# Kernel optimization log

Measured on AMD Instinct MI355X. Metric: run time of the kernel, lower is better.

The kernel has to match this reference:

```python
import jax, jax.numpy as jnp
import numpy as np

B, CIN, COUT, K, NS, NIN, H = 4, 128, 128, 9, 16384, 16384, 64
W0 = 30.0  # SIREN first-layer frequency


def setup_inputs() -> dict:
    ks = jax.random.split(jax.random.key(0), 8)
    x = jax.random.normal(ks[0], (B, CIN, NIN), dtype=jnp.float32)
    neighbours = jax.random.randint(ks[1], (K, NS), 0, NIN)
    # normalized relative neighbour coordinates in [-1, 1], shape (K*NS, 2)
    coords = 2.0 * jax.random.uniform(ks[2], (K * NS, 2), dtype=jnp.float32) - 1.0
    W1 = jax.random.normal(ks[3], (2, H), dtype=jnp.float32) / jnp.sqrt(2.0)
    b1 = jnp.zeros((H,), dtype=jnp.float32)
    W2 = jax.random.normal(ks[4], (H, H), dtype=jnp.float32) / jnp.sqrt(H * 1.0)
    b2 = jnp.zeros((H,), dtype=jnp.float32)
    W3 = jax.random.normal(ks[5], (H, COUT * CIN), dtype=jnp.float32) / jnp.sqrt(H * 1.0)
    b3 = jnp.zeros((COUT * CIN,), dtype=jnp.float32)
    bias = jnp.zeros((1, COUT, 1), dtype=jnp.float32)
    return {"x": x, "neighbours": neighbours, "coords": coords,
            "W1": W1, "b1": b1, "W2": W2, "b2": b2, "W3": W3, "b3": b3,
            "bias": bias}


def reference(x, neighbours, coords, W1, b1, W2, b2, W3, b3, bias):
    k, ns = neighbours.shape
    cin = x.shape[1]
    cout = W3.shape[1] // cin
    # INR filter generation: (K*NS, 2) -> (K*NS, COUT*CIN)
    h = jnp.sin(W0 * (coords @ W1 + b1))
    h = jnp.sin(h @ W2 + b2)
    f = h @ W3 + b3                                  # (K*NS, COUT*CIN)
    # (K*NS, COUT, CIN) -> (COUT, CIN, K, NS), matching torch permute(1,2,0).reshape
    f = f.reshape(k * ns, cout, cin).transpose(1, 2, 0).reshape(cout, cin, k, ns)
    # neighbor gather: (B, CIN, K, NS)
    x_unfold = x[:, :, neighbours]
    # weighted reduce over (CIN, K) per output location
    out = jnp.einsum('bjkl,ijkl->bil', x_unfold, f)
    return out + bias
```

## Files before the change

### kernel.cpp

```cpp
#include <hip/hip_runtime.h>

#define NS   16384
#define NIN  16384
#define CIN  128
#define COUT 128
#define KNB  9
#define MCH  66
#define QDIM (CIN*MCH)
#define W0C  30.0f

typedef __bf16 bf16;
typedef bf16  bf16x8  __attribute__((ext_vector_type(8)));
typedef bf16  bf16x2  __attribute__((ext_vector_type(2)));
typedef unsigned short u16;
typedef u16   u16x8   __attribute__((ext_vector_type(8)));
typedef float floatx4 __attribute__((ext_vector_type(4)));
typedef unsigned int u32;

__device__ inline u16 f2bf(float f){
  u32 u = __float_as_uint(f);
  u += 0x7fffu + ((u >> 16) & 1u);
  return (u16)(u >> 16);
}
__device__ inline float bf2f(u16 s){
  return __uint_as_float((u32)s << 16);
}
__device__ inline u32 cvtpk2(float lo, float hi){
  u32 r; asm("v_cvt_pk_bf16_f32 %0, %1, %2" : "=v"(r) : "v"(lo), "v"(hi)); return r;
}

#if defined(__has_builtin)
# if __has_builtin(__builtin_amdgcn_fdot2_f32_bf16)
#  define HAVE_DOT2 1
# endif
#endif
#ifndef HAVE_DOT2
# define HAVE_DOT2 0
#endif

__device__ inline float dot2bf(u32 x2, u32 h2, float c){
#if HAVE_DOT2
  return __builtin_amdgcn_fdot2_f32_bf16(__builtin_bit_cast(bf16x2, x2),
                                         __builtin_bit_cast(bf16x2, h2), c, false);
#else
  float xl = bf2f((u16)(x2 & 0xffffu)), xh = bf2f((u16)(x2 >> 16));
  float hl = bf2f((u16)(h2 & 0xffffu)), hh = bf2f((u16)(h2 >> 16));
  return fmaf(xh, hh, fmaf(xl, hl, c));
#endif
}

#define WG_BARRIER() do { \
  asm volatile("s_waitcnt lgkmcnt(0)" ::: "memory"); \
  __builtin_amdgcn_s_barrier(); \
} while (0)

#define PREP_K1H  (NS/32)
#define PREP_KTR  2048
#define PREP_K0   ((COUT*QDIM + 1023)/1024)
__global__ __launch_bounds__(1024) void k_prep(
      const float* __restrict__ coords,
      const float* __restrict__ W1, const float* __restrict__ b1,
      const float* __restrict__ W2, const float* __restrict__ b2,
      const float* __restrict__ x,
      const float* __restrict__ W3, const float* __restrict__ b3,
      u32* __restrict__ hK, u16* __restrict__ xT, u16* __restrict__ Vt){
  __shared__ u16 sh[KNB][32][66];
  __shared__ __align__(16) float tfl[4][32][33];
  const int bid = blockIdx.x;
  const int tid = threadIdx.x;

  if (bid < PREP_K1H){
    const int lane = tid & 63;
    const int w    = tid >> 6;
    const int l0   = bid*32;
    for (int e = w; e < KNB*32; e += 16){
      int k = e >> 5, l = e & 31;
      int pt = (k << 14) + l0 + l;
      float c0 = coords[2*pt], c1 = coords[2*pt+1];
      float z  = fmaf(c0, W1[lane], fmaf(c1, W1[64+lane], b1[lane]));
      float h1 = sinf(W0C * z);
      float acc = b2[lane];
      #pragma unroll
      for (int mp = 0; mp < 64; ++mp)
        acc = fmaf(__shfl(h1, mp, 64), W2[mp*64 + lane], acc);
      sh[k][l][lane] = f2bf(sinf(acc));
      if (lane == 0){ sh[k][l][64] = 0x3F80; sh[k][l][65] = 0; }
    }
    __syncthreads();
    for (int e = tid; e < 66*5*32; e += 1024){
      int m  = e / 160;
      int r  = e - m*160;
      int kp = r >> 5;
      int l  = r & 31;
      u32 lo = sh[2*kp][l][m];
      u32 hi = (kp < 4) ? (u32)sh[2*kp+1][l][m] : 0u;
      hK[(((size_t)m*5 + kp) << 14) + l0 + l] = lo | (hi << 16);
    }
  } else if (bid < PREP_K1H + PREP_KTR){
    const int sub = tid >> 8;
    const int tx  = tid & 31;
    const int ty  = (tid >> 5) & 7;
    const int t   = (bid - PREP_K1H)*4 + sub;
    const int p0  = (t & 511) * 32;
    const int j0  = ((t >> 9) & 3) * 32;
    const int b   = t >> 11;
    const float* xb  = x  + (size_t)b*CIN*NIN;
    u16*         xTb = xT + (size_t)b*NIN*CIN;
    #pragma unroll
    for (int n = 0; n < 4; ++n)
      tfl[sub][ty+8*n][tx] = xb[(size_t)(j0+ty+8*n)*NIN + p0+tx];
    __syncthreads();
    #pragma unroll
    for (int n = 0; n < 4; ++n)
      xTb[(size_t)(p0+ty+8*n)*CIN + j0+tx] = f2bf(tfl[sub][tx][ty+8*n]);
  } else {
    int idx = (bid - PREP_K1H - PREP_KTR)*1024 + tid;
    if (idx < COUT*QDIM){
      int i = idx / QDIM;
      int q = idx - i*QDIM;
      int m = q >> 7;
      int j = q & 127;
      float v = 0.f;
      if (m < 64)       v = W3[m*16384 + i*128 + j];
      else if (m == 64) v = b3[i*128 + j];
      Vt[idx] = f2bf(v);
    }
  }
}

__global__ __launch_bounds__(512, 4) void k_fused(
      const u16* __restrict__ xT,
      const u32* __restrict__ hK,
      const int* __restrict__ nb,
      const u16* __restrict__ Vt,
      const float* __restrict__ bias,
      float* __restrict__ out){
  __shared__ __align__(16) u16 A[2][2][32][136];
  __shared__ u32 hs[2][2][5][32];
  __shared__ int pk[KNB][32];

  const int tid = threadIdx.x;
  const int r0  = blockIdx.x * 32;
  const int b   = r0 >> 14;
  const int l0  = r0 & (NS-1);

  if (tid < KNB*32){
    int k = tid >> 5, l = tid & 31;
    pk[k][l] = nb[k*NS + l0 + l];
  }
  WG_BARRIER();

  const int lq = tid >> 4;
  const int jc = tid & 15;

  const bool hact = tid < 320;
  const int  hs_  = tid / 160;
  const int  hr_  = tid - hs_*160;
  const int  hkp_ = hr_ >> 5;
  const int  hl_  = hr_ & 31;
  const u32* hKp  = hK + (((size_t)(5*hs_ + hkp_)) << 14) + l0 + hl_;
  const size_t HSTR = (size_t)10 << 14;
  u32 hra = 0, hrb = 0;
  if (hact){
    u32 h0 = hKp[0];
    hra = hKp[HSTR];
    hrb = hKp[2*HSTR];
    hs[0][hs_][hkp_][hl_] = h0;
  }

  const char* xbB = (const char*)(xT + ((size_t)b << 21));
  u32 xp[5][8];
  #pragma unroll
  for (int kp = 0; kp < 4; ++kp){
    u16x8 ga = *(const u16x8*)(xbB + (((size_t)(u32)pk[2*kp  ][lq]) << 8) + (size_t)jc*16);
    u16x8 gb = *(const u16x8*)(xbB + (((size_t)(u32)pk[2*kp+1][lq]) << 8) + (size_t)jc*16);
    #pragma unroll
    for (int j = 0; j < 8; ++j) xp[kp][j] = (u32)ga[j] | ((u32)gb[j] << 16);
  }
  {
    u16x8 ga = *(const u16x8*)(xbB + (((size_t)(u32)pk[8][lq]) << 8) + (size_t)jc*16);
    #pragma unroll
    for (int j = 0; j < 8; ++j) xp[4][j] = (u32)ga[j];
  }

  const int lane  = tid & 63;
  const int w     = tid >> 6;
  const int iq    = w & 3;
  const int kh    = w >> 2;
  const int ar    = lane & 15;
  const int klane = lane >> 4;

  floatx4 acc[2][2];
  #pragma unroll
  for (int r = 0; r < 2; ++r)
    #pragma unroll
    for (int f = 0; f < 2; ++f)
      acc[r][f] = (floatx4){0.f,0.f,0.f,0.f};

  const char* VtB0 = (const char*)Vt + (size_t)(iq*32      + ar)*(QDIM*2) + (size_t)(kh*128 + klane*16);
  const char* VtB1 = (const char*)Vt + (size_t)(iq*32 + 16 + ar)*(QDIM*2) + (size_t)(kh*128 + klane*16);

  bf16x8 bv[2][4];
  #pragma unroll
  for (int mm = 0; mm < 2; ++mm)
    #pragma unroll
    for (int kt = 0; kt < 2; ++kt){
      bv[0][mm*2+kt] = *(const bf16x8*)(VtB0 + mm*256 + kt*64);
      bv[1][mm*2+kt] = *(const bf16x8*)(VtB1 + mm*256 + kt*64);
    }

  WG_BARRIER();

  for (int mg = 0; mg < 33; ++mg){
    const int pb = mg & 1;

    float a2[2][8];
    #pragma unroll
    for (int s = 0; s < 2; ++s)
      #pragma unroll
      for (int j = 0; j < 8; ++j) a2[s][j] = 0.f;
    #pragma unroll
    for (int s = 0; s < 2; ++s){
      #pragma unroll
      for (int kp = 0; kp < 5; ++kp){
        u32 hp = hs[pb][s][kp][lq];
        #pragma unroll
        for (int j = 0; j < 8; ++j)
          a2[s][j] = dot2bf(xp[kp][j], hp, a2[s][j]);
      }
    }
    {
      uint4 q0, q1;
      q0.x = cvtpk2(a2[0][0], a2[0][1]); q0.y = cvtpk2(a2[0][2], a2[0][3]);
      q0.z = cvtpk2(a2[0][4], a2[0][5]); q0.w = cvtpk2(a2[0][6], a2[0][7]);
      q1.x = cvtpk2(a2[1][0], a2[1][1]); q1.y = cvtpk2(a2[1][2], a2[1][3]);
      q1.z = cvtpk2(a2[1][4], a2[1][5]); q1.w = cvtpk2(a2[1][6], a2[1][7]);
      *(uint4*)&A[pb][0][lq][jc*8] = q0;
      *(uint4*)&A[pb][1][lq][jc*8] = q1;
    }

    if (hact){
      if (mg < 32) hs[pb^1][hs_][hkp_][hl_] = hra;
      hra = hrb;
      if (mg <= 29) hrb = hKp[(size_t)(mg+3)*HSTR];
    }

    WG_BARRIER();

    #pragma unroll
    for (int mm = 0; mm < 2; ++mm){
      const char* Ab = (const char*)&A[pb][mm][0][0] + kh*128 + klane*16;
      #pragma unroll
      for (int kt = 0; kt < 2; ++kt){
        bf16x8 av0 = *(const bf16x8*)(Ab + (     ar)*272 + kt*64);
        bf16x8 av1 = *(const bf16x8*)(Ab + (16 + ar)*272 + kt*64);
        acc[0][0] = __builtin_amdgcn_mfma_f32_16x16x32_bf16(av0, bv[0][mm*2+kt], acc[0][0], 0, 0, 0);
        acc[0][1] = __builtin_amdgcn_mfma_f32_16x16x32_bf16(av0, bv[1][mm*2+kt], acc[0][1], 0, 0, 0);
        acc[1][0] = __builtin_amdgcn_mfma_f32_16x16x32_bf16(av1, bv[0][mm*2+kt], acc[1][0], 0, 0, 0);
        acc[1][1] = __builtin_amdgcn_mfma_f32_16x16x32_bf16(av1, bv[1][mm*2+kt], acc[1][1], 0, 0, 0);
      }
    }

    if (mg < 32){
      const char* Vg0 = VtB0 + (size_t)(mg+1)*512;
      const char* Vg1 = VtB1 + (size_t)(mg+1)*512;
      #pragma unroll
      for (int mm = 0; mm < 2; ++mm)
        #pragma unroll
        for (int kt = 0; kt < 2; ++kt){
          bv[0][mm*2+kt] = *(const bf16x8*)(Vg0 + mm*256 + kt*64);
          bv[1][mm*2+kt] = *(const bf16x8*)(Vg1 + mm*256 + kt*64);
        }
    }
  }

  WG_BARRIER();
  floatx4* red = (floatx4*)&A[0][0][0][0];
  if (kh == 1){
    floatx4* dst = red + (((size_t)iq*64 + lane) << 2);
    dst[0] = acc[0][0]; dst[1] = acc[0][1]; dst[2] = acc[1][0]; dst[3] = acc[1][1];
  }
  WG_BARRIER();
  if (kh == 0){
    const floatx4* src = red + (((size_t)iq*64 + lane) << 2);
    acc[0][0] += src[0]; acc[0][1] += src[1];
    acc[1][0] += src[2]; acc[1][1] += src[3];
    float* ob = out + ((size_t)b << 21);
    #pragma unroll
    for (int rf = 0; rf < 2; ++rf){
      #pragma unroll
      for (int f = 0; f < 2; ++f){
        int i = iq*32 + f*16 + ar;
        float bi = bias[i];
        int l = l0 + rf*16 + klane*4;
        float4 v;
        v.x = acc[rf][f][0] + bi;
        v.y = acc[rf][f][1] + bi;
        v.z = acc[rf][f][2] + bi;
        v.w = acc[rf][f][3] + bi;
        *(float4*)(ob + ((size_t)i << 14) + l) = v;
      }
    }
  }
}

__global__ __launch_bounds__(256) void k_naive(const float* __restrict__ x,
      const int* __restrict__ nb, const float* __restrict__ coords,
      const float* __restrict__ W1, const float* __restrict__ b1,
      const float* __restrict__ W2, const float* __restrict__ b2,
      const float* __restrict__ W3, const float* __restrict__ b3,
      const float* __restrict__ bias, float* __restrict__ out){
  __shared__ __align__(16) float hk[KNB][68];
  __shared__ int pk[KNB];
  __shared__ __align__(16) float xg[4][KNB][128];
  __shared__ __align__(16) float ul[128][66];
  int tid = threadIdx.x;
  int l = blockIdx.x;
  int lane = tid & 63, wid = tid >> 6;
  if (tid < KNB) pk[tid] = nb[tid*NS + l];
  for (int k = wid; k < KNB; k += 4){
    int pt = k*NS + l;
    float c0 = coords[2*pt], c1 = coords[2*pt+1];
    float z  = fmaf(c0, W1[lane], fmaf(c1, W1[64+lane], b1[lane]));
    float h1 = sinf(W0C*z);
    float a = b2[lane];
    for (int mp = 0; mp < 64; ++mp)
      a = fmaf(__shfl(h1, mp, 64), W2[mp*64+lane], a);
    hk[k][lane] = sinf(a);
    if (lane == 0){ hk[k][64] = 1.f; hk[k][65] = 0.f; }
  }
  __syncthreads();
  for (int idx = tid; idx < 4*KNB*128; idx += 256){
    int b = idx / (KNB*128);
    int r = idx - b*KNB*128;
    int k = r >> 7;
    int j = r & 127;
    xg[b][k][j] = x[((size_t)b*CIN + j)*NIN + pk[k]];
  }
  __syncthreads();
  for (int b = 0; b < 4; ++b){
    for (int idx = tid; idx < 128*65; idx += 256){
      int j = idx / 65, m = idx - j*65;
      float s = 0.f;
      for (int k = 0; k < KNB; ++k) s = fmaf(xg[b][k][j], hk[k][m], s);
      ul[j][m] = s;
    }
    __syncthreads();
    if (tid < 128){
      int i = tid;
      float v = bias[i];
      for (int j = 0; j < 128; ++j){
        const float* wcol = W3 + i*128 + j;
        for (int m = 0; m < 64; ++m)
          v = fmaf(ul[j][m], wcol[(size_t)m*16384], v);
        v = fmaf(ul[j][64], b3[i*128+j], v);
      }
      out[((size_t)b<<21) + ((size_t)i<<14) + l] = v;
    }
    __syncthreads();
  }
}

extern "C" void kernel_launch(void* const* d_in, const int* in_sizes, int n_in,
                              void* d_out, int out_size, void* d_ws, size_t ws_size,
                              hipStream_t stream) {
  const float* x      = (const float*)d_in[0];
  const int*   nb     = (const int*)  d_in[1];
  const float* coords = (const float*)d_in[2];
  const float* W1     = (const float*)d_in[3];
  const float* b1     = (const float*)d_in[4];
  const float* W2     = (const float*)d_in[5];
  const float* b2     = (const float*)d_in[6];
  const float* W3     = (const float*)d_in[7];
  const float* b3     = (const float*)d_in[8];
  const float* bias   = (const float*)d_in[9];
  float* out = (float*)d_out;

  const size_t VT_BYTES = (size_t)COUT*QDIM*2;
  const size_t HK_BYTES = (size_t)MCH*5*NS*4;
  const size_t XT_BYTES = (size_t)4*NIN*CIN*2;
  const size_t FIXED    = VT_BYTES + HK_BYTES + XT_BYTES;

  if (ws_size >= FIXED) {
    char* ws = (char*)d_ws;
    unsigned short* Vt = (unsigned short*)ws;
    u32*            hK = (u32*)(ws + VT_BYTES);
    unsigned short* xT = (unsigned short*)(ws + VT_BYTES + HK_BYTES);

    k_prep<<<PREP_K1H + PREP_KTR + PREP_K0, 1024, 0, stream>>>(
        coords, W1, b1, W2, b2, x, W3, b3, hK, xT, Vt);
    k_fused<<<(4*NS)/32, 512, 0, stream>>>(xT, hK, nb, Vt, bias, out);
  } else {
    k_naive<<<NS, 256, 0, stream>>>(x, nb, coords, W1, b1, W2, b2, W3, b3, bias, out);
  }
  (void)in_sizes; (void)n_in; (void)out_size;
}
```

Baseline: 687.7 us.

## Process two m-groups per barrier to halve workgroup synchronizations

The main loop now handles two m-groups per iteration, with double-buffered LDS tiles for A and hs that each hold two sub-stages. This halves the number of workgroup barriers, from 33 to 17. The hK prefetch is restructured to load pairs of rows, and the Vt register prefetch is split between the two MFMA sub-phases. The cost is twice the LDS for A and hs, which may reduce occupancy, and some awkward index logic, such as clamping rr1 and the final Vt load at the end of the loop, which may read past valid data.

```diff
diff --git a/kernel.cpp b/kernel.cpp
--- a/kernel.cpp
+++ b/kernel.cpp
@@ -135,8 +135,8 @@
       const u16* __restrict__ Vt,
       const float* __restrict__ bias,
       float* __restrict__ out){
-  __shared__ __align__(16) u16 A[2][2][32][136];
-  __shared__ u32 hs[2][2][5][32];
+  __shared__ __align__(16) u16 A[2][2][2][32][136];
+  __shared__ u32 hs[2][2][2][5][32];
   __shared__ int pk[KNB][32];
 
   const int tid = threadIdx.x;
@@ -159,13 +159,16 @@
   const int  hkp_ = hr_ >> 5;
   const int  hl_  = hr_ & 31;
   const u32* hKp  = hK + (((size_t)(5*hs_ + hkp_)) << 14) + l0 + hl_;
-  const size_t HSTR = (size_t)10 << 14;
-  u32 hra = 0, hrb = 0;
+  u32 hra[2] = {0,0}, hrb[2] = {0,0};
   if (hact){
-    u32 h0 = hKp[0];
-    hra = hKp[HSTR];
-    hrb = hKp[2*HSTR];
-    hs[0][hs_][hkp_][hl_] = h0;
+    u32 h00 = hKp[(size_t)( 0) << 14];
+    u32 h01 = hKp[(size_t)(10) << 14];
+    hra[0]  = hKp[(size_t)(20) << 14];
+    hra[1]  = hKp[(size_t)(30) << 14];
+    hrb[0]  = hKp[(size_t)(40) << 14];
+    hrb[1]  = hKp[(size_t)(50) << 14];
+    hs[0][0][hs_][hkp_][hl_] = h00;
+    hs[0][1][hs_][hkp_][hl_] = h01;
   }
 
   const char* xbB = (const char*)(xT + ((size_t)b << 21));
@@ -211,45 +214,57 @@
 
   WG_BARRIER();
 
-  for (int mg = 0; mg < 33; ++mg){
-    const int pb = mg & 1;
-
-    float a2[2][8];
-    #pragma unroll
-    for (int s = 0; s < 2; ++s)
-      #pragma unroll
-      for (int j = 0; j < 8; ++j) a2[s][j] = 0.f;
-    #pragma unroll
-    for (int s = 0; s < 2; ++s){
-      #pragma unroll
-      for (int kp = 0; kp < 5; ++kp){
-        u32 hp = hs[pb][s][kp][lq];
+  for (int it = 0; it < 17; ++it){
+    const int pb = it & 1;
+
+    #pragma unroll
+    for (int sub = 0; sub < 2; ++sub){
+      if (2*it + sub < 33){
+        float a2[2][8];
         #pragma unroll
-        for (int j = 0; j < 8; ++j)
-          a2[s][j] = dot2bf(xp[kp][j], hp, a2[s][j]);
-      }
-    }
-    {
-      uint4 q0, q1;
-      q0.x = cvtpk2(a2[0][0], a2[0][1]); q0.y = cvtpk2(a2[0][2], a2[0][3]);
-      q0.z = cvtpk2(a2[0][4], a2[0][5]); q0.w = cvtpk2(a2[0][6], a2[0][7]);
-      q1.x = cvtpk2(a2[1][0], a2[1][1]); q1.y = cvtpk2(a2[1][2], a2[1][3]);
-      q1.z = cvtpk2(a2[1][4], a2[1][5]); q1.w = cvtpk2(a2[1][6], a2[1][7]);
-      *(uint4*)&A[pb][0][lq][jc*8] = q0;
-      *(uint4*)&A[pb][1][lq][jc*8] = q1;
+        for (int s = 0; s < 2; ++s)
+          #pragma unroll
+          for (int j = 0; j < 8; ++j) a2[s][j] = 0.f;
+        #pragma unroll
+        for (int s = 0; s < 2; ++s){
+          #pragma unroll
+          for (int kp = 0; kp < 5; ++kp){
+            u32 hp = hs[pb][sub][s][kp][lq];
+            #pragma unroll
+            for (int j = 0; j < 8; ++j)
+              a2[s][j] = dot2bf(xp[kp][j], hp, a2[s][j]);
+          }
+        }
+        uint4 q0, q1;
+        q0.x = cvtpk2(a2[0][0], a2[0][1]); q0.y = cvtpk2(a2[0][2], a2[0][3]);
+        q0.z = cvtpk2(a2[0][4], a2[0][5]); q0.w = cvtpk2(a2[0][6], a2[0][7]);
+        q1.x = cvtpk2(a2[1][0], a2[1][1]); q1.y = cvtpk2(a2[1][2], a2[1][3]);
+        q1.z = cvtpk2(a2[1][4], a2[1][5]); q1.w = cvtpk2(a2[1][6], a2[1][7]);
+        *(uint4*)&A[pb][sub][0][lq][jc*8] = q0;
+        *(uint4*)&A[pb][sub][1][lq][jc*8] = q1;
+      }
     }
 
     if (hact){
-      if (mg < 32) hs[pb^1][hs_][hkp_][hl_] = hra;
-      hra = hrb;
-      if (mg <= 29) hrb = hKp[(size_t)(mg+3)*HSTR];
+      if (it < 16){
+        hs[pb^1][0][hs_][hkp_][hl_] = hra[0];
+        hs[pb^1][1][hs_][hkp_][hl_] = hra[1];
+      }
+      hra[0] = hrb[0]; hra[1] = hrb[1];
+      if (it + 3 <= 16){
+        int rr0 = (it+3)*20;
+        int rr1 = rr0 + 10;
+        if (rr1 > 320) rr1 = 0;
+        hrb[0] = hKp[(size_t)rr0 << 14];
+        hrb[1] = hKp[(size_t)rr1 << 14];
+      }
     }
 
     WG_BARRIER();
 
     #pragma unroll
     for (int mm = 0; mm < 2; ++mm){
-      const char* Ab = (const char*)&A[pb][mm][0][0] + kh*128 + klane*16;
+      const char* Ab = (const char*)&A[pb][0][mm][0][0] + kh*128 + klane*16;
       #pragma unroll
       for (int kt = 0; kt < 2; ++kt){
         bf16x8 av0 = *(const bf16x8*)(Ab + (     ar)*272 + kt*64);
@@ -261,9 +276,9 @@
       }
     }
 
-    if (mg < 32){
-      const char* Vg0 = VtB0 + (size_t)(mg+1)*512;
-      const char* Vg1 = VtB1 + (size_t)(mg+1)*512;
+    {
+      const char* Vg0 = VtB0 + (size_t)(2*it + 1)*512;
+      const char* Vg1 = VtB1 + (size_t)(2*it + 1)*512;
       #pragma unroll
       for (int mm = 0; mm < 2; ++mm)
         #pragma unroll
@@ -272,10 +287,35 @@
           bv[1][mm*2+kt] = *(const bf16x8*)(Vg1 + mm*256 + kt*64);
         }
     }
+
+    if (it < 16){
+      #pragma unroll
+      for (int mm = 0; mm < 2; ++mm){
+        const char* Ab = (const char*)&A[pb][1][mm][0][0] + kh*128 + klane*16;
+        #pragma unroll
+        for (int kt = 0; kt < 2; ++kt){
+          bf16x8 av0 = *(const bf16x8*)(Ab + (     ar)*272 + kt*64);
+          bf16x8 av1 = *(const bf16x8*)(Ab + (16 + ar)*272 + kt*64);
+          acc[0][0] = __builtin_amdgcn_mfma_f32_16x16x32_bf16(av0, bv[0][mm*2+kt], acc[0][0], 0, 0, 0);
+          acc[0][1] = __builtin_amdgcn_mfma_f32_16x16x32_bf16(av0, bv[1][mm*2+kt], acc[0][1], 0, 0, 0);
+          acc[1][0] = __builtin_amdgcn_mfma_f32_16x16x32_bf16(av1, bv[0][mm*2+kt], acc[1][0], 0, 0, 0);
+          acc[1][1] = __builtin_amdgcn_mfma_f32_16x16x32_bf16(av1, bv[1][mm*2+kt], acc[1][1], 0, 0, 0);
+        }
+      }
+      const char* Vg0 = VtB0 + (size_t)(2*it + 2)*512;
+      const char* Vg1 = VtB1 + (size_t)(2*it + 2)*512;
+      #pragma unroll
+      for (int mm = 0; mm < 2; ++mm)
+        #pragma unroll
+        for (int kt = 0; kt < 2; ++kt){
+          bv[0][mm*2+kt] = *(const bf16x8*)(Vg0 + mm*256 + kt*64);
+          bv[1][mm*2+kt] = *(const bf16x8*)(Vg1 + mm*256 + kt*64);
+        }
+    }
   }
 
   WG_BARRIER();
-  floatx4* red = (floatx4*)&A[0][0][0][0];
+  floatx4* red = (floatx4*)&A[0][0][0][0][0];
   if (kh == 1){
     floatx4* dst = red + (((size_t)iq*64 + lane) << 2);
     dst[0] = acc[0][0]; dst[1] = acc[0][1]; dst[2] = acc[1][0]; dst[3] = acc[1][1];
```

New measurement: 694.1 us. About the same (+0.9%).
